# Performance work log

Hardware: AMD Instinct MI355X
Metric: run time of the kernel (lower is better)

The kernel has to match this reference:

```python
import jax, jax.numpy as jnp
import numpy as np

L, D, H, N, R = 4, 256, 512, 16, 8  # layers, d_model, hidden=2*d_model, state_dim, dt_rank
OUT_LEN, IN_DIM = 96, 32
EPS = 1e-5


def _layernorm(v, g, b):
    m = jnp.mean(v, axis=-1, keepdims=True)
    var = jnp.mean((v - m) ** 2, axis=-1, keepdims=True)
    return (v - m) / jnp.sqrt(var + EPS) * g + b


def _pos_encoding(T, d):
    pos = jnp.arange(T, dtype=jnp.float32)[:, None]
    div = jnp.exp(jnp.arange(0, d, 2, dtype=jnp.float32) * (-np.log(10000.0) / d))
    pe = jnp.zeros((T, d), dtype=jnp.float32)
    pe = pe.at[:, 0::2].set(jnp.sin(pos * div))
    pe = pe.at[:, 1::2].set(jnp.cos(pos * div))
    return pe


def setup_inputs() -> dict:
    key = jax.random.key(0)
    ks = jax.random.split(key, 20)
    inp = {
        "x": jax.random.normal(ks[0], (8, 1024, IN_DIM), dtype=jnp.float32),
        "emb_w": jax.random.normal(ks[1], (D, IN_DIM), dtype=jnp.float32) * 0.1,
        "emb_b": jnp.zeros((D,), dtype=jnp.float32),
        "norm_g": jnp.ones((L, D), dtype=jnp.float32),
        "norm_b": jnp.zeros((L, D), dtype=jnp.float32),
        "in_w": jax.random.normal(ks[2], (L, H, D), dtype=jnp.float32) * (1.0 / np.sqrt(D)),
        "conv_w": jax.random.normal(ks[3], (L, H, 1, 3), dtype=jnp.float32) * 0.5,
        "A_p": jax.random.normal(ks[4], (L, H, N), dtype=jnp.float32) * 0.01,
        "D_p": jnp.ones((L, H), dtype=jnp.float32),
        "dt1_w": jax.random.normal(ks[5], (L, R, H), dtype=jnp.float32) * (1.0 / np.sqrt(H)),
        "dt1_b": jnp.zeros((L, R), dtype=jnp.float32),
        "dt2_w": jax.random.normal(ks[6], (L, H, R), dtype=jnp.float32) * (1.0 / np.sqrt(R)),
        "dt2_b": jnp.zeros((L, H), dtype=jnp.float32),
        "out_w": jax.random.normal(ks[7], (L, D, H), dtype=jnp.float32) * (1.0 / np.sqrt(H)),
        "final_g": jnp.ones((D,), dtype=jnp.float32),
        "final_b": jnp.zeros((D,), dtype=jnp.float32),
        "head1_w": jax.random.normal(ks[8], (D, D), dtype=jnp.float32) * (1.0 / np.sqrt(D)),
        "head1_b": jnp.zeros((D,), dtype=jnp.float32),
        "head2_w": jax.random.normal(ks[9], (OUT_LEN, D), dtype=jnp.float32) * (1.0 / np.sqrt(D)),
        "head2_b": jnp.zeros((OUT_LEN,), dtype=jnp.float32),
    }
    return inp


def _mamba_block(h, g, b, in_w, conv_w, A_p, D_p, dt1_w, dt1_b, dt2_w, dt2_b, out_w):
    res = h
    v = _layernorm(h, g, b)            # [B,T,D]
    v = jnp.einsum('btd,hd->bth', v, in_w)  # [B,T,H]
    # depthwise conv1d, kernel 3, padding 1, groups=H
    vc = jnp.transpose(v, (0, 2, 1))   # [B,H,T]
    vc = jax.lax.conv_general_dilated(vc, conv_w, window_strides=(1,),
                                      padding=[(1, 1)], feature_group_count=H,
                                      dimension_numbers=('NCH', 'OIH', 'NCH'))
    v = jnp.transpose(jax.nn.silu(vc), (0, 2, 1))  # [B,T,H]
    dt = jax.nn.relu(jnp.einsum('bth,rh->btr', v, dt1_w) + dt1_b)
    dt = jnp.einsum('btr,hr->bth', dt, dt2_w) + dt2_b
    dt = jax.nn.softplus(dt)           # [B,T,H]
    A = -jnp.exp(A_p)                  # [H,N]
    safe_A = jnp.where(jnp.abs(A) < 1e-5, jnp.ones_like(A), A)

    B_sz = v.shape[0]
    state0 = jnp.zeros((B_sz, H, N), dtype=v.dtype)

    def step(state, inp):
        x_t, dt_t = inp  # [B,H] each
        dA = A * dt_t[..., None]            # [B,H,N]
        discA = jnp.exp(dA)
        discB = (discA - 1.0) / safe_A * dt_t[..., None]
        state = discA * state + discB * x_t[..., None]
        y = jnp.einsum('bhn,hn->bh', state, A_p) + D_p * x_t
        return state, y

    xs = (jnp.transpose(v, (1, 0, 2)), jnp.transpose(dt, (1, 0, 2)))  # [T,B,H]
    _, ys = jax.lax.scan(step, state0, xs)
    y = jnp.transpose(ys, (1, 0, 2))   # [B,T,H]
    return res + jnp.einsum('bth,dh->btd', y, out_w)


def reference(x, emb_w, emb_b, norm_g, norm_b, in_w, conv_w, A_p, D_p,
              dt1_w, dt1_b, dt2_w, dt2_b, out_w, final_g, final_b,
              head1_w, head1_b, head2_w, head2_b):
    h = jnp.einsum('bti,di->btd', x, emb_w) + emb_b  # [B,T,D]
    h = h + _pos_encoding(h.shape[1], D)[None]
    for l in range(L):
        h = _mamba_block(h, norm_g[l], norm_b[l], in_w[l], conv_w[l], A_p[l],
                         D_p[l], dt1_w[l], dt1_b[l], dt2_w[l], dt2_b[l], out_w[l])
    h = _layernorm(h, final_g, final_b)
    h = h[:, -1, :]                    # last token [B,D]
    h = jax.nn.silu(h @ head1_w.T + head1_b)
    return h @ head2_w.T + head2_b     # [B, OUT_LEN]
```

## Files before the change

### kernel.cpp

```cpp
#include <hip/hip_runtime.h>
#include <hip/hip_bf16.h>
#include <math.h>

#define BB 8
#define TT 1024
#define DD 256
#define HH 512
#define NN 16
#define RR 8
#define OUT_LEN 96
#define IN_DIM 32
#define MM (BB*TT)

#define SC 16
#define CC (TT/SC)

typedef unsigned short u16;
typedef unsigned int u32;
typedef __attribute__((ext_vector_type(8))) short short8;
typedef __attribute__((ext_vector_type(8))) unsigned short u16x8;
typedef __attribute__((ext_vector_type(4))) float float4v;

__device__ __forceinline__ u16 f2bf(float f) {
    __hip_bfloat16 h = __float2bfloat16(f);
    return *(u16*)&h;
}
__device__ __forceinline__ float bf2f(u16 u) {
    u32 v = ((u32)u) << 16;
    return *(float*)&v;
}

#define GLD_LDS16(src, dst) __builtin_amdgcn_global_load_lds( \
    (const __attribute__((address_space(1))) void*)(src),     \
    (__attribute__((address_space(3))) void*)(dst), 16, 0, 0)

__global__ __launch_bounds__(256) void embed_ln_cvt_kernel(
    const float* __restrict__ x, const float* __restrict__ emb_w,
    const float* __restrict__ emb_b,
    const float* __restrict__ g, const float* __restrict__ b,
    float* __restrict__ h, u16* __restrict__ lnout,
    const float* __restrict__ w_in, u16* __restrict__ wbf_in,
    const float* __restrict__ w_out, u16* __restrict__ wbf_out, int nw)
{
    int bid = blockIdx.x;
    if (bid >= MM) {
        int i = (bid - MM) * 256 + threadIdx.x;
        if (i < nw) wbf_in[i] = f2bf(w_in[i]);
        else        wbf_out[i - nw] = f2bf(w_out[i - nw]);
        return;
    }

    int bt = bid;
    int d  = threadIdx.x;
    int t  = bt & (TT - 1);

    __shared__ float xs[IN_DIM];
    __shared__ float red[4], red2[4];
    if (threadIdx.x < IN_DIM) xs[threadIdx.x] = x[bt * IN_DIM + threadIdx.x];
    __syncthreads();

    const float* w = emb_w + d * IN_DIM;
    float acc = emb_b[d];
#pragma unroll
    for (int i = 0; i < IN_DIM; i++) acc = fmaf(xs[i], w[i], acc);

    int i2 = d & ~1;
    float div = __expf(-(float)i2 * 0.0359778918f);
    float arg = (float)t * div;
    float pe = (d & 1) ? __cosf(arg) : __sinf(arg);
    float val = acc + pe;
    h[bt * DD + d] = val;

    float s = val;
#pragma unroll
    for (int o = 32; o > 0; o >>= 1) s += __shfl_down(s, o);
    int lane = d & 63, wave = d >> 6;
    if (lane == 0) red[wave] = s;
    __syncthreads();
    float mean = (red[0] + red[1] + red[2] + red[3]) * (1.0f / DD);

    float c = val - mean;
    float s2 = c * c;
#pragma unroll
    for (int o = 32; o > 0; o >>= 1) s2 += __shfl_down(s2, o);
    if (lane == 0) red2[wave] = s2;
    __syncthreads();
    float var = (red2[0] + red2[1] + red2[2] + red2[3]) * (1.0f / DD);

    lnout[bt * DD + d] = f2bf(c * rsqrtf(var + 1e-5f) * g[d] + b[d]);
}

template<int BM, int BN, int OUT_BF16>
__global__ __launch_bounds__(256) void gemm_bf16(
    const u16* __restrict__ A, const u16* __restrict__ B,
    void* __restrict__ Cv, int M, int N, int K, int addC)
{
    constexpr int BK = 64;
    constexpr int MT = BM / 32;
    constexpr int NT = BN / 32;
    static_assert(BN == 64, "B staging assumes BN==64");

    __shared__ __align__(16) u16 Al[2][8][BM][8];
    __shared__ __align__(16) u16 Bl[2][8][BN][8];

    const int tid = threadIdx.x;
    const int bm = blockIdx.y * BM;
    const int bn = blockIdx.x * BN;
    const int wid = tid >> 6, lane = tid & 63;
    const int wm = wid >> 1, wn = wid & 1;
    const int lq = lane >> 4, lm = lane & 15;

    float4v acc[MT][NT];
#pragma unroll
    for (int i = 0; i < MT; i++)
#pragma unroll
        for (int j = 0; j < NT; j++) acc[i][j] = (float4v){0.f, 0.f, 0.f, 0.f};

#pragma unroll
    for (int it = 0; it < (8 * BM) / 256; it++) {
        int c = it * 256 + tid;
        int q = c / BM, row = c % BM;
        GLD_LDS16(A + (size_t)(bm + row) * K + q * 8, &Al[0][q][row][0]);
    }
#pragma unroll
    for (int it = 0; it < (8 * BN) / 256; it++) {
        int c = it * 256 + tid;
        int q = c / BN, row = c % BN;
        GLD_LDS16(B + (size_t)(bn + row) * K + q * 8, &Bl[0][q][row][0]);
    }
    __syncthreads();

    int cur = 0;
    for (int k0 = 0; k0 < K; k0 += BK) {
        if (k0 + BK < K) {
            int nxt = cur ^ 1;
#pragma unroll
            for (int it = 0; it < (8 * BM) / 256; it++) {
                int c = it * 256 + tid;
                int q = c / BM, row = c % BM;
                GLD_LDS16(A + (size_t)(bm + row) * K + k0 + BK + q * 8, &Al[nxt][q][row][0]);
            }
#pragma unroll
            for (int it = 0; it < (8 * BN) / 256; it++) {
                int c = it * 256 + tid;
                int q = c / BN, row = c % BN;
                GLD_LDS16(B + (size_t)(bn + row) * K + k0 + BK + q * 8, &Bl[nxt][q][row][0]);
            }
        }

        short8 af[2][MT], bf[2][NT];
#pragma unroll
        for (int kk = 0; kk < 2; kk++) {
#pragma unroll
            for (int mt = 0; mt < MT; mt++)
                af[kk][mt] = *(const short8*)&Al[cur][kk * 4 + lq][wm * (BM / 2) + mt * 16 + lm][0];
#pragma unroll
            for (int nt = 0; nt < NT; nt++)
                bf[kk][nt] = *(const short8*)&Bl[cur][kk * 4 + lq][wn * (BN / 2) + nt * 16 + lm][0];
        }

#pragma unroll
        for (int kk = 0; kk < 2; kk++)
#pragma unroll
            for (int mt = 0; mt < MT; mt++)
#pragma unroll
                for (int nt = 0; nt < NT; nt++)
                    acc[mt][nt] = __builtin_amdgcn_mfma_f32_16x16x32_bf16(
                        af[kk][mt], bf[kk][nt], acc[mt][nt], 0, 0, 0);
        __syncthreads();
        cur ^= 1;
    }

#pragma unroll
    for (int mt = 0; mt < MT; mt++)
#pragma unroll
        for (int nt = 0; nt < NT; nt++) {
            int row0 = bm + wm * (BM / 2) + mt * 16 + lq * 4;
            int col  = bn + wn * (BN / 2) + nt * 16 + lm;
#pragma unroll
            for (int r = 0; r < 4; r++) {
                float vv = acc[mt][nt][r];
                if (OUT_BF16) {
                    ((u16*)Cv)[(size_t)(row0 + r) * N + col] = f2bf(vv);
                } else {
                    float* cp = (float*)Cv + (size_t)(row0 + r) * N + col;
                    if (addC) vv += *cp;
                    *cp = vv;
                }
            }
        }
}

__global__ __launch_bounds__(256) void gemm2_ln(
    const u16* __restrict__ A, const u16* __restrict__ B,
    float* __restrict__ h,
    const float* __restrict__ g, const float* __restrict__ bb,
    u16* __restrict__ lnout, int doLN)
{
    constexpr int BM = 32;
    __shared__ __align__(16) u16 Al[2][8][BM][8];
    __shared__ __align__(16) u16 Bl[2][8][256][8];
    __shared__ float rs[2][BM], qs[2][BM];

    const int tid = threadIdx.x;
    const int bm = blockIdx.x * BM;
    const int wid = tid >> 6, lane = tid & 63;
    const int wm = wid >> 1, wn = wid & 1;
    const int lq = lane >> 4, lm = lane & 15;

    float4v acc[8];
#pragma unroll
    for (int j = 0; j < 8; j++) acc[j] = (float4v){0.f, 0.f, 0.f, 0.f};

    {
        int q = tid >> 5, row = tid & 31;
        GLD_LDS16(A + (size_t)(bm + row) * 512 + q * 8, &Al[0][q][row][0]);
    }
#pragma unroll
    for (int it = 0; it < 8; it++) {
        int c = it * 256 + tid;
        int q = c >> 8, row = c & 255;
        GLD_LDS16(B + (size_t)row * 512 + q * 8, &Bl[0][q][row][0]);
    }
    __syncthreads();

    int cur = 0;
    for (int k0 = 0; k0 < 512; k0 += 64) {
        if (k0 + 64 < 512) {
            int nxt = cur ^ 1;
            {
                int q = tid >> 5, row = tid & 31;
                GLD_LDS16(A + (size_t)(bm + row) * 512 + k0 + 64 + q * 8, &Al[nxt][q][row][0]);
            }
#pragma unroll
            for (int it = 0; it < 8; it++) {
                int c = it * 256 + tid;
                int q = c >> 8, row = c & 255;
                GLD_LDS16(B + (size_t)row * 512 + k0 + 64 + q * 8, &Bl[nxt][q][row][0]);
            }
        }

        short8 af[2], bf[2][8];
#pragma unroll
        for (int kk = 0; kk < 2; kk++) {
            af[kk] = *(const short8*)&Al[cur][kk * 4 + lq][wm * 16 + lm][0];
#pragma unroll
            for (int nt = 0; nt < 8; nt++)
                bf[kk][nt] = *(const short8*)&Bl[cur][kk * 4 + lq][wn * 128 + nt * 16 + lm][0];
        }
#pragma unroll
        for (int kk = 0; kk < 2; kk++)
#pragma unroll
            for (int nt = 0; nt < 8; nt++)
                acc[nt] = __builtin_amdgcn_mfma_f32_16x16x32_bf16(
                    af[kk], bf[kk][nt], acc[nt], 0, 0, 0);
        __syncthreads();
        cur ^= 1;
    }

    float val[4][8];
    float s1[4] = {0.f, 0.f, 0.f, 0.f}, s2[4] = {0.f, 0.f, 0.f, 0.f};
#pragma unroll
    for (int r = 0; r < 4; r++) {
        int row = bm + wm * 16 + lq * 4 + r;
#pragma unroll
        for (int nt = 0; nt < 8; nt++) {
            int col = wn * 128 + nt * 16 + lm;
            float v = acc[nt][r] + h[(size_t)row * DD + col];
            val[r][nt] = v;
            s1[r] += v;
            s2[r] = fmaf(v, v, s2[r]);
            h[(size_t)row * DD + col] = v;
        }
    }
#pragma unroll
    for (int r = 0; r < 4; r++) {
#pragma unroll
        for (int o = 1; o < 16; o <<= 1) {
            s1[r] += __shfl_xor(s1[r], o);
            s2[r] += __shfl_xor(s2[r], o);
        }
    }
    if (lm == 0) {
#pragma unroll
        for (int r = 0; r < 4; r++) {
            rs[wn][wm * 16 + lq * 4 + r] = s1[r];
            qs[wn][wm * 16 + lq * 4 + r] = s2[r];
        }
    }
    __syncthreads();

    if (doLN) {
#pragma unroll
        for (int r = 0; r < 4; r++) {
            int i = wm * 16 + lq * 4 + r;
            int row = bm + i;
            float mean = (rs[0][i] + rs[1][i]) * (1.0f / DD);
            float var  = (qs[0][i] + qs[1][i]) * (1.0f / DD) - mean * mean;
            float rstd = rsqrtf(var + 1e-5f);
#pragma unroll
            for (int nt = 0; nt < 8; nt++) {
                int col = wn * 128 + nt * 16 + lm;
                lnout[(size_t)row * DD + col] =
                    f2bf((val[r][nt] - mean) * rstd * g[col] + bb[col]);
            }
        }
    }
}

__global__ __launch_bounds__(256) void conv_dt1_kernel(
    const u16* __restrict__ v, const float* __restrict__ cwg,
    const float* __restrict__ w1g, const float* __restrict__ b1g,
    u16* __restrict__ vsb, float* __restrict__ dtr)
{
    __shared__ float w1s[RR * 2 * 256];
    int tid = threadIdx.x;
    {
        int lane = tid & 63, rc = tid >> 6;
#pragma unroll
        for (int i = 0; i < 4; i++) {
            int rci = rc + i * 4;
            int r = rci >> 1, jc = rci & 1;
            float4 wv = *(const float4*)(w1g + r * HH + lane * 8 + jc * 4);
            *(float4*)&w1s[rci * 256 + lane * 4] = wv;
        }
    }
    __syncthreads();

    int wave = tid >> 6, lane = tid & 63;
    int m = blockIdx.x * 4 + wave;
    int t = m & (TT - 1);
    int h0 = lane * 8;

    const u16* vrow = v + (size_t)m * HH + h0;
    u16x8 x0 = *(const u16x8*)vrow;
    u16x8 xm = (t > 0)      ? *(const u16x8*)(vrow - HH) : (u16x8)(0);
    u16x8 xp = (t < TT - 1) ? *(const u16x8*)(vrow + HH) : (u16x8)(0);

    const float* wp = cwg + h0 * 3;
    float a[8];
    u16x8 o;
#pragma unroll
    for (int j = 0; j < 8; j++) {
        float s = wp[j * 3] * bf2f(xm[j]);
        s = fmaf(wp[j * 3 + 1], bf2f(x0[j]), s);
        s = fmaf(wp[j * 3 + 2], bf2f(xp[j]), s);
        s = s / (1.0f + __expf(-s));
        a[j] = s;
        o[j] = f2bf(s);
    }
    *(u16x8*)(vsb + (size_t)m * HH + h0) = o;

    float acc[RR];
#pragma unroll
    for (int r = 0; r < RR; r++) {
        float4 wlo = *(const float4*)&w1s[(r * 2 + 0) * 256 + lane * 4];
        float4 whi = *(const float4*)&w1s[(r * 2 + 1) * 256 + lane * 4];
        float s = a[0] * wlo.x;
        s = fmaf(a[1], wlo.y, s);
        s = fmaf(a[2], wlo.z, s);
        s = fmaf(a[3], wlo.w, s);
        s = fmaf(a[4], whi.x, s);
        s = fmaf(a[5], whi.y, s);
        s = fmaf(a[6], whi.z, s);
        s = fmaf(a[7], whi.w, s);
        acc[r] = s;
    }
#pragma unroll
    for (int r = 0; r < RR; r++) {
#pragma unroll
        for (int o2 = 1; o2 < 64; o2 <<= 1) acc[r] += __shfl_xor(acc[r], o2);
    }
    if (lane == 0) {
#pragma unroll
        for (int r = 0; r < RR; r++) acc[r] = fmaxf(acc[r] + b1g[r], 0.0f);
        *(float4*)(dtr + (size_t)m * RR)     = make_float4(acc[0], acc[1], acc[2], acc[3]);
        *(float4*)(dtr + (size_t)m * RR + 4) = make_float4(acc[4], acc[5], acc[6], acc[7]);
    }
}

__device__ __forceinline__ float softplus_f(float s) {
    return (s > 20.0f) ? s : __logf(1.0f + __expf(s));
}

__global__ __launch_bounds__(256, 4) void scan_pass1(
    const u16* __restrict__ vs, const float* __restrict__ dtr,
    const float* __restrict__ dt2_w, const float* __restrict__ dt2_b,
    const float* __restrict__ A_p,
    u16* __restrict__ Lst, float* __restrict__ sdt)
{
    int h = blockIdx.x * 256 + threadIdx.x;
    int c = blockIdx.y;
    int b = blockIdx.z;

    __shared__ float ds[SC * RR];
    {
        const float* drow = dtr + ((size_t)b * TT + (size_t)c * SC) * RR;
        if (threadIdx.x < SC * RR) ds[threadIdx.x] = drow[threadIdx.x];
    }

    float A2[NN], invA[NN], st[NN];
    const float* ap = A_p + h * NN;
#pragma unroll
    for (int n = 0; n < NN; n++) {
        float a = -__expf(ap[n]);
        A2[n] = a * 1.44269504f;
        invA[n] = 1.0f / a;
        st[n] = 0.0f;
    }
    float w2[RR];
#pragma unroll
    for (int r = 0; r < RR; r++) w2[r] = dt2_w[h * RR + r];
    float b2 = dt2_b[h];

    const u16* vbase = vs + ((size_t)b * TT + (size_t)c * SC) * HH + h;
    float xv = bf2f(vbase[0]);
    __syncthreads();

    float s_dt = 0.0f;
#pragma unroll 2
    for (int t = 0; t < SC; t++) {
        float xn = (t + 1 < SC) ? bf2f(vbase[(size_t)(t + 1) * HH]) : 0.0f;
        float s = b2;
#pragma unroll
        for (int r = 0; r < RR; r++) s = fmaf(ds[t * RR + r], w2[r], s);
        float dt = softplus_f(s);
        s_dt += dt;
        float dtx = dt * xv;
#pragma unroll
        for (int n = 0; n < NN; n++) {
            float e = __builtin_amdgcn_exp2f(A2[n] * dt);
            float u = invA[n] * dtx;
            st[n] = fmaf(e, st[n] + u, -u);
        }
        xv = xn;
    }

    size_t base = (((size_t)c * BB + b) * HH + h) * NN;
    u16x8 lo, hi;
#pragma unroll
    for (int n = 0; n < 8; n++) { lo[n] = f2bf(st[n]); hi[n] = f2bf(st[n + 8]); }
    *(u16x8*)(Lst + base)     = lo;
    *(u16x8*)(Lst + base + 8) = hi;
    sdt[((size_t)c * BB + b) * HH + h] = s_dt;
}

__global__ __launch_bounds__(256) void scan_carry_par(
    const float* __restrict__ A_p, const float* __restrict__ sdt,
    u16* __restrict__ Lst)
{
    int gw   = (blockIdx.x << 2) | (threadIdx.x >> 6);
    int lane = threadIdx.x & 63;
    int b = gw >> 9;
    int h = gw & 511;

    size_t sidx = ((size_t)lane * BB + b) * HH + h;
    float sd = sdt[sidx];
    const float* ap = A_p + h * NN;
    u16x8 Llo = *(const u16x8*)(Lst + sidx * NN);
    u16x8 Lhi = *(const u16x8*)(Lst + sidx * NN + 8);
    u16x8 Elo, Ehi;
#pragma unroll
    for (int n = 0; n < NN; n++) {
        float An = -__expf(ap[n]);
        float p  = __expf(An * sd);
        float lv = bf2f((n < 8) ? Llo[n] : Lhi[n - 8]);
#pragma unroll
        for (int d2 = 1; d2 < 64; d2 <<= 1) {
            float pp = __shfl_up(p, d2);
            float pl = __shfl_up(lv, d2);
            if (lane >= d2) { lv = fmaf(pl, p, lv); p = pp * p; }
        }
        float E = __shfl_up(lv, 1);
        if (lane == 0) E = 0.0f;
        if (n < 8) Elo[n] = f2bf(E); else Ehi[n - 8] = f2bf(E);
    }
    *(u16x8*)(Lst + sidx * NN)     = Elo;
    *(u16x8*)(Lst + sidx * NN + 8) = Ehi;
}

__global__ __launch_bounds__(256, 4) void scan_pass2(
    const u16* __restrict__ vs,
    const float* __restrict__ dtr,
    const float* __restrict__ dt2_w,
    const float* __restrict__ dt2_b,
    const float* __restrict__ A_p, const float* __restrict__ D_p,
    const u16* __restrict__ carry,
    u16* __restrict__ y)
{
    int h = blockIdx.x * 256 + threadIdx.x;
    int c = blockIdx.y;
    int b = blockIdx.z;

    __shared__ float ds[SC * RR];
    {
        const float* drow = dtr + ((size_t)b * TT + (size_t)c * SC) * RR;
        if (threadIdx.x < SC * RR) ds[threadIdx.x] = drow[threadIdx.x];
    }

    float A2[NN], invA[NN], Ap[NN], st[NN];
    const float* app = A_p + h * NN;
    size_t cbase = (((size_t)c * BB + b) * HH + h) * NN;
    {
        u16x8 lo = *(const u16x8*)(carry + cbase);
        u16x8 hi = *(const u16x8*)(carry + cbase + 8);
#pragma unroll
        for (int n = 0; n < 8; n++) { st[n] = bf2f(lo[n]); st[n + 8] = bf2f(hi[n]); }
    }
#pragma unroll
    for (int n = 0; n < NN; n++) {
        float apv = app[n];
        Ap[n] = apv;
        float a = -__expf(apv);
        A2[n] = a * 1.44269504f;
        invA[n] = 1.0f / a;
    }
    float w2[RR];
#pragma unroll
    for (int r = 0; r < RR; r++) w2[r] = dt2_w[h * RR + r];
    float b2 = dt2_b[h];
    float Dp = D_p[h];

    const u16* vbase = vs + ((size_t)b * TT + (size_t)c * SC) * HH + h;
    u16*       ybase = y  + ((size_t)b * TT + (size_t)c * SC) * HH + h;
    float xv = bf2f(vbase[0]);
    __syncthreads();

#pragma unroll 2
    for (int t = 0; t < SC; t++) {
        float xn = (t + 1 < SC) ? bf2f(vbase[(size_t)(t + 1) * HH]) : 0.0f;
        float s = b2;
#pragma unroll
        for (int r = 0; r < RR; r++) s = fmaf(ds[t * RR + r], w2[r], s);
        float dt = softplus_f(s);
        float dtx = dt * xv;
        float acc = Dp * xv;
#pragma unroll
        for (int n = 0; n < NN; n++) {
            float e = __builtin_amdgcn_exp2f(A2[n] * dt);
            float u = invA[n] * dtx;
            st[n] = fmaf(e, st[n] + u, -u);
            acc = fmaf(st[n], Ap[n], acc);
        }
        ybase[(size_t)t * HH] = f2bf(acc);
        xv = xn;
    }
}

__global__ __launch_bounds__(256) void head_kernel(
    const float* __restrict__ h,
    const float* __restrict__ fg, const float* __restrict__ fb,
    const float* __restrict__ w1, const float* __restrict__ b1,
    const float* __restrict__ w2, const float* __restrict__ b2,
    float* __restrict__ out)
{
    int b = blockIdx.x;
    int d = threadIdx.x;
    __shared__ float hn[DD], s1[DD];
    __shared__ float red[4];

    float v = h[((size_t)b * TT + (TT - 1)) * DD + d];

    float s = v;
#pragma unroll
    for (int o = 32; o > 0; o >>= 1) s += __shfl_down(s, o);
    int lane = d & 63, wave = d >> 6;
    if (lane == 0) red[wave] = s;
    __syncthreads();
    float mean = (red[0] + red[1] + red[2] + red[3]) * (1.0f / DD);
    __syncthreads();

    float c = v - mean;
    float s2 = c * c;
#pragma unroll
    for (int o = 32; o > 0; o >>= 1) s2 += __shfl_down(s2, o);
    if (lane == 0) red[wave] = s2;
    __syncthreads();
    float var = (red[0] + red[1] + red[2] + red[3]) * (1.0f / DD);

    hn[d] = c * rsqrtf(var + 1e-5f) * fg[d] + fb[d];
    __syncthreads();

    float a1 = b1[d];
    const float* w1r = w1 + d * DD;
#pragma unroll 8
    for (int k = 0; k < DD; k++) a1 = fmaf(hn[k], w1r[k], a1);
    s1[d] = a1 / (1.0f + __expf(-a1));
    __syncthreads();

    if (d < OUT_LEN) {
        float a2 = b2[d];
        const float* w2r = w2 + d * DD;
#pragma unroll 8
        for (int k = 0; k < DD; k++) a2 = fmaf(s1[k], w2r[k], a2);
        out[b * OUT_LEN + d] = a2;
    }
}

extern "C" void kernel_launch(void* const* d_in, const int* in_sizes, int n_in,
                              void* d_out, int out_size, void* d_ws, size_t ws_size,
                              hipStream_t stream)
{
    (void)in_sizes; (void)n_in; (void)out_size; (void)ws_size;

    const float* x       = (const float*)d_in[0];
    const float* emb_w   = (const float*)d_in[1];
    const float* emb_b   = (const float*)d_in[2];
    const float* norm_g  = (const float*)d_in[3];
    const float* norm_b  = (const float*)d_in[4];
    const float* in_w    = (const float*)d_in[5];
    const float* conv_w  = (const float*)d_in[6];
    const float* A_p     = (const float*)d_in[7];
    const float* D_p     = (const float*)d_in[8];
    const float* dt1_w   = (const float*)d_in[9];
    const float* dt1_b   = (const float*)d_in[10];
    const float* dt2_w   = (const float*)d_in[11];
    const float* dt2_b   = (const float*)d_in[12];
    const float* out_w   = (const float*)d_in[13];
    const float* final_g = (const float*)d_in[14];
    const float* final_b = (const float*)d_in[15];
    const float* head1_w = (const float*)d_in[16];
    const float* head1_b = (const float*)d_in[17];
    const float* head2_w = (const float*)d_in[18];
    const float* head2_b = (const float*)d_in[19];
    float* outp = (float*)d_out;

    char* ws = (char*)d_ws;
    float* h     = (float*)ws;                ws += (size_t)MM * DD * 4;
    u16*   vbf   = (u16*)ws;                  ws += (size_t)MM * HH * 2;
    u16*   vsb   = (u16*)ws;                  ws += (size_t)MM * HH * 2;
    u16*   ybf   = (u16*)ws;                  ws += (size_t)MM * HH * 2;
    u16*   lnbuf = (u16*)ws;                  ws += (size_t)MM * DD * 2;
    float* dtr   = (float*)ws;                ws += (size_t)MM * RR * 4;
    u16*   Lst   = (u16*)ws;                  ws += (size_t)CC * BB * HH * NN * 2;
    float* sdt   = (float*)ws;                ws += (size_t)CC * BB * HH * 4;
    u16*   wbf_in  = (u16*)ws;                ws += (size_t)4 * HH * DD * 2;
    u16*   wbf_out = (u16*)ws;                ws += (size_t)4 * DD * HH * 2;

    const int NW = 4 * HH * DD;
    embed_ln_cvt_kernel<<<MM + (2 * NW) / 256, 256, 0, stream>>>(
        x, emb_w, emb_b, norm_g, norm_b, h, lnbuf,
        in_w, wbf_in, out_w, wbf_out, NW);

    for (int l = 0; l < 4; l++) {
        gemm_bf16<128, 64, 1><<<dim3(HH / 64, MM / 128), 256, 0, stream>>>(
            lnbuf, wbf_in + (size_t)l * HH * DD, vbf, MM, HH, DD, 0);
        conv_dt1_kernel<<<MM / 4, 256, 0, stream>>>(
            vbf, conv_w + (size_t)l * HH * 3,
            dt1_w + (size_t)l * RR * HH, dt1_b + l * RR, vsb, dtr);

        scan_pass1<<<dim3(HH / 256, CC, BB), 256, 0, stream>>>(
            vsb, dtr, dt2_w + (size_t)l * HH * RR, dt2_b + l * HH,
            A_p + (size_t)l * HH * NN, Lst, sdt);
        scan_carry_par<<<(BB * HH) / 4, 256, 0, stream>>>(
            A_p + (size_t)l * HH * NN, sdt, Lst);
        scan_pass2<<<dim3(HH / 256, CC, BB), 256, 0, stream>>>(
            vsb, dtr, dt2_w + (size_t)l * HH * RR, dt2_b + l * HH,
            A_p + (size_t)l * HH * NN, D_p + l * HH, Lst, ybf);

        const float* g_next = (l < 3) ? (norm_g + (l + 1) * DD) : final_g;
        const float* b_next = (l < 3) ? (norm_b + (l + 1) * DD) : final_b;
        gemm2_ln<<<MM / 32, 256, 0, stream>>>(
            ybf, wbf_out + (size_t)l * DD * HH, h, g_next, b_next,
            lnbuf, (l < 3) ? 1 : 0);
    }

    head_kernel<<<BB, 256, 0, stream>>>(h, final_g, final_b,
                                        head1_w, head1_b, head2_w, head2_b, outp);
}
```

Baseline: 498.8 us.

## Fuse conv/dt1 into scan pass1 and use vmcnt-based waits in GEMMs

Merges the depthwise conv + SiLU + dt1 projection kernel into the first chunked-scan pass. Each 512-thread block now computes one chunk's conv outputs and stages them in LDS, so the scan reads its inputs from LDS instead of global memory, and one launch is removed per layer. Separately, both GEMM kernels replace __syncthreads with explicit s_waitcnt vmcnt(N) plus s_barrier, so the next tile's loads can stay in flight while the current tile is consumed. The hardcoded vmcnt counts tie the GEMM code to specific tile shapes. The fused kernel also runs only 64x8 blocks of 512 threads, which lowers parallelism for the conv part.

New measurement: 485.7 us. 2.6% less time.

```diff
diff --git a/kernel.cpp b/kernel.cpp
--- a/kernel.cpp
+++ b/kernel.cpp
@@ -34,6 +34,11 @@
     (const __attribute__((address_space(1))) void*)(src),     \
     (__attribute__((address_space(3))) void*)(dst), 16, 0, 0)
 
+#define SBAR()   asm volatile("s_barrier" ::: "memory")
+#define VMCNT0() asm volatile("s_waitcnt vmcnt(0)" ::: "memory")
+#define VMCNT6() asm volatile("s_waitcnt vmcnt(6)" ::: "memory")
+#define VMCNT9() asm volatile("s_waitcnt vmcnt(9)" ::: "memory")
+
 __global__ __launch_bounds__(256) void embed_ln_cvt_kernel(
     const float* __restrict__ x, const float* __restrict__ emb_w,
     const float* __restrict__ emb_b,
@@ -98,7 +103,7 @@
     constexpr int BK = 64;
     constexpr int MT = BM / 32;
     constexpr int NT = BN / 32;
-    static_assert(BN == 64, "B staging assumes BN==64");
+    static_assert(BM == 128 && BN == 64, "vmcnt count assumes 6 loads/thread");
 
     __shared__ __align__(16) u16 Al[2][8][BM][8];
     __shared__ __align__(16) u16 Bl[2][8][BN][8];
@@ -128,25 +133,30 @@
         int q = c / BN, row = c % BN;
         GLD_LDS16(B + (size_t)(bn + row) * K + q * 8, &Bl[0][q][row][0]);
     }
-    __syncthreads();
-
+
+    const int nt = K / BK;
     int cur = 0;
-    for (int k0 = 0; k0 < K; k0 += BK) {
-        if (k0 + BK < K) {
+    for (int i = 0; i < nt; i++) {
+        if (i + 1 < nt) {
             int nxt = cur ^ 1;
+            int k1 = (i + 1) * BK;
 #pragma unroll
             for (int it = 0; it < (8 * BM) / 256; it++) {
                 int c = it * 256 + tid;
                 int q = c / BM, row = c % BM;
-                GLD_LDS16(A + (size_t)(bm + row) * K + k0 + BK + q * 8, &Al[nxt][q][row][0]);
+                GLD_LDS16(A + (size_t)(bm + row) * K + k1 + q * 8, &Al[nxt][q][row][0]);
             }
 #pragma unroll
             for (int it = 0; it < (8 * BN) / 256; it++) {
                 int c = it * 256 + tid;
                 int q = c / BN, row = c % BN;
-                GLD_LDS16(B + (size_t)(bn + row) * K + k0 + BK + q * 8, &Bl[nxt][q][row][0]);
+                GLD_LDS16(B + (size_t)(bn + row) * K + k1 + q * 8, &Bl[nxt][q][row][0]);
             }
-        }
+            VMCNT6();
+        } else {
+            VMCNT0();
+        }
+        SBAR();
 
         short8 af[2][MT], bf[2][NT];
 #pragma unroll
@@ -155,8 +165,8 @@
             for (int mt = 0; mt < MT; mt++)
                 af[kk][mt] = *(const short8*)&Al[cur][kk * 4 + lq][wm * (BM / 2) + mt * 16 + lm][0];
 #pragma unroll
-            for (int nt = 0; nt < NT; nt++)
-                bf[kk][nt] = *(const short8*)&Bl[cur][kk * 4 + lq][wn * (BN / 2) + nt * 16 + lm][0];
+            for (int nt2 = 0; nt2 < NT; nt2++)
+                bf[kk][nt2] = *(const short8*)&Bl[cur][kk * 4 + lq][wn * (BN / 2) + nt2 * 16 + lm][0];
         }
 
 #pragma unroll
@@ -164,22 +174,22 @@
 #pragma unroll
             for (int mt = 0; mt < MT; mt++)
 #pragma unroll
-                for (int nt = 0; nt < NT; nt++)
-                    acc[mt][nt] = __builtin_amdgcn_mfma_f32_16x16x32_bf16(
-                        af[kk][mt], bf[kk][nt], acc[mt][nt], 0, 0, 0);
-        __syncthreads();
+                for (int nt2 = 0; nt2 < NT; nt2++)
+                    acc[mt][nt2] = __builtin_amdgcn_mfma_f32_16x16x32_bf16(
+                        af[kk][mt], bf[kk][nt2], acc[mt][nt2], 0, 0, 0);
+        SBAR();
         cur ^= 1;
     }
 
 #pragma unroll
     for (int mt = 0; mt < MT; mt++)
 #pragma unroll
-        for (int nt = 0; nt < NT; nt++) {
+        for (int nt2 = 0; nt2 < NT; nt2++) {
             int row0 = bm + wm * (BM / 2) + mt * 16 + lq * 4;
-            int col  = bn + wn * (BN / 2) + nt * 16 + lm;
+            int col  = bn + wn * (BN / 2) + nt2 * 16 + lm;
 #pragma unroll
             for (int r = 0; r < 4; r++) {
-                float vv = acc[mt][nt][r];
+                float vv = acc[mt][nt2][r];
                 if (OUT_BF16) {
                     ((u16*)Cv)[(size_t)(row0 + r) * N + col] = f2bf(vv);
                 } else {
@@ -222,23 +232,27 @@
         int q = c >> 8, row = c & 255;
         GLD_LDS16(B + (size_t)row * 512 + q * 8, &Bl[0][q][row][0]);
     }
-    __syncthreads();
 
     int cur = 0;
-    for (int k0 = 0; k0 < 512; k0 += 64) {
-        if (k0 + 64 < 512) {
+    for (int i = 0; i < 8; i++) {
+        if (i + 1 < 8) {
             int nxt = cur ^ 1;
+            int k1 = (i + 1) * 64;
             {
                 int q = tid >> 5, row = tid & 31;
-                GLD_LDS16(A + (size_t)(bm + row) * 512 + k0 + 64 + q * 8, &Al[nxt][q][row][0]);
+                GLD_LDS16(A + (size_t)(bm + row) * 512 + k1 + q * 8, &Al[nxt][q][row][0]);
             }
 #pragma unroll
             for (int it = 0; it < 8; it++) {
                 int c = it * 256 + tid;
                 int q = c >> 8, row = c & 255;
-                GLD_LDS16(B + (size_t)row * 512 + k0 + 64 + q * 8, &Bl[nxt][q][row][0]);
+                GLD_LDS16(B + (size_t)row * 512 + k1 + q * 8, &Bl[nxt][q][row][0]);
             }
-        }
+            VMCNT9();
+        } else {
+            VMCNT0();
+        }
+        SBAR();
 
         short8 af[2], bf[2][8];
 #pragma unroll
@@ -254,7 +268,7 @@
             for (int nt = 0; nt < 8; nt++)
                 acc[nt] = __builtin_amdgcn_mfma_f32_16x16x32_bf16(
                     af[kk], bf[kk][nt], acc[nt], 0, 0, 0);
-        __syncthreads();
+        SBAR();
         cur ^= 1;
     }
 
@@ -308,104 +322,102 @@
     }
 }
 
-__global__ __launch_bounds__(256) void conv_dt1_kernel(
-    const u16* __restrict__ v, const float* __restrict__ cwg,
-    const float* __restrict__ w1g, const float* __restrict__ b1g,
-    u16* __restrict__ vsb, float* __restrict__ dtr)
-{
-    __shared__ float w1s[RR * 2 * 256];
-    int tid = threadIdx.x;
-    {
-        int lane = tid & 63, rc = tid >> 6;
-#pragma unroll
-        for (int i = 0; i < 4; i++) {
-            int rci = rc + i * 4;
-            int r = rci >> 1, jc = rci & 1;
-            float4 wv = *(const float4*)(w1g + r * HH + lane * 8 + jc * 4);
-            *(float4*)&w1s[rci * 256 + lane * 4] = wv;
-        }
-    }
-    __syncthreads();
-
-    int wave = tid >> 6, lane = tid & 63;
-    int m = blockIdx.x * 4 + wave;
-    int t = m & (TT - 1);
-    int h0 = lane * 8;
-
-    const u16* vrow = v + (size_t)m * HH + h0;
-    u16x8 x0 = *(const u16x8*)vrow;
-    u16x8 xm = (t > 0)      ? *(const u16x8*)(vrow - HH) : (u16x8)(0);
-    u16x8 xp = (t < TT - 1) ? *(const u16x8*)(vrow + HH) : (u16x8)(0);
-
-    const float* wp = cwg + h0 * 3;
-    float a[8];
-    u16x8 o;
-#pragma unroll
-    for (int j = 0; j < 8; j++) {
-        float s = wp[j * 3] * bf2f(xm[j]);
-        s = fmaf(wp[j * 3 + 1], bf2f(x0[j]), s);
-        s = fmaf(wp[j * 3 + 2], bf2f(xp[j]), s);
-        s = s / (1.0f + __expf(-s));
-        a[j] = s;
-        o[j] = f2bf(s);
-    }
-    *(u16x8*)(vsb + (size_t)m * HH + h0) = o;
-
-    float acc[RR];
-#pragma unroll
-    for (int r = 0; r < RR; r++) {
-        float4 wlo = *(const float4*)&w1s[(r * 2 + 0) * 256 + lane * 4];
-        float4 whi = *(const float4*)&w1s[(r * 2 + 1) * 256 + lane * 4];
-        float s = a[0] * wlo.x;
-        s = fmaf(a[1], wlo.y, s);
-        s = fmaf(a[2], wlo.z, s);
-        s = fmaf(a[3], wlo.w, s);
-        s = fmaf(a[4], whi.x, s);
-        s = fmaf(a[5], whi.y, s);
-        s = fmaf(a[6], whi.z, s);
-        s = fmaf(a[7], whi.w, s);
-        acc[r] = s;
-    }
-#pragma unroll
-    for (int r = 0; r < RR; r++) {
-#pragma unroll
-        for (int o2 = 1; o2 < 64; o2 <<= 1) acc[r] += __shfl_xor(acc[r], o2);
-    }
-    if (lane == 0) {
-#pragma unroll
-        for (int r = 0; r < RR; r++) acc[r] = fmaxf(acc[r] + b1g[r], 0.0f);
-        *(float4*)(dtr + (size_t)m * RR)     = make_float4(acc[0], acc[1], acc[2], acc[3]);
-        *(float4*)(dtr + (size_t)m * RR + 4) = make_float4(acc[4], acc[5], acc[6], acc[7]);
-    }
-}
-
 __device__ __forceinline__ float softplus_f(float s) {
     return (s > 20.0f) ? s : __logf(1.0f + __expf(s));
 }
 
-__global__ __launch_bounds__(256, 4) void scan_pass1(
-    const u16* __restrict__ vs, const float* __restrict__ dtr,
+__global__ __launch_bounds__(512, 4) void conv_scan1(
+    const u16* __restrict__ vbf, const float* __restrict__ cwg,
+    const float* __restrict__ w1g, const float* __restrict__ b1g,
     const float* __restrict__ dt2_w, const float* __restrict__ dt2_b,
     const float* __restrict__ A_p,
+    u16* __restrict__ vsb, float* __restrict__ dtr,
     u16* __restrict__ Lst, float* __restrict__ sdt)
 {
-    int h = blockIdx.x * 256 + threadIdx.x;
-    int c = blockIdx.y;
-    int b = blockIdx.z;
-
+    const int c = blockIdx.x;
+    const int b = blockIdx.y;
+    const int tid = threadIdx.x;
+    const int wave = tid >> 6, lane = tid & 63;
+    const int h0 = lane * 8;
+
+    __shared__ float w1s[RR * 2 * 256];
+    __shared__ u16   a_lds[SC][HH];
     __shared__ float ds[SC * RR];
-    {
-        const float* drow = dtr + ((size_t)b * TT + (size_t)c * SC) * RR;
-        if (threadIdx.x < SC * RR) ds[threadIdx.x] = drow[threadIdx.x];
-    }
-
+
+#pragma unroll
+    for (int i = 0; i < 2; i++) {
+        int rci = wave + i * 8;
+        int r = rci >> 1, jc = rci & 1;
+        float4 wv = *(const float4*)(w1g + r * HH + lane * 8 + jc * 4);
+        *(float4*)&w1s[rci * 256 + lane * 4] = wv;
+    }
+    __syncthreads();
+
+    const float* wp = cwg + h0 * 3;
+#pragma unroll
+    for (int i = 0; i < 2; i++) {
+        int tr = wave + i * 8;
+        int t  = c * SC + tr;
+        size_t m = (size_t)b * TT + t;
+
+        const u16* vrow = vbf + m * HH + h0;
+        u16x8 x0 = *(const u16x8*)vrow;
+        u16x8 xm = (t > 0)      ? *(const u16x8*)(vrow - HH) : (u16x8)(0);
+        u16x8 xp = (t < TT - 1) ? *(const u16x8*)(vrow + HH) : (u16x8)(0);
+
+        float a[8];
+        u16x8 o;
+#pragma unroll
+        for (int j = 0; j < 8; j++) {
+            float s = wp[j * 3] * bf2f(xm[j]);
+            s = fmaf(wp[j * 3 + 1], bf2f(x0[j]), s);
+            s = fmaf(wp[j * 3 + 2], bf2f(xp[j]), s);
+            s = s / (1.0f + __expf(-s));
+            a[j] = s;
+            o[j] = f2bf(s);
+        }
+        *(u16x8*)(vsb + m * HH + h0) = o;
+        *(u16x8*)&a_lds[tr][h0]      = o;
+
+        float acc[RR];
+#pragma unroll
+        for (int r = 0; r < RR; r++) {
+            float4 wlo = *(const float4*)&w1s[(r * 2 + 0) * 256 + lane * 4];
+            float4 whi = *(const float4*)&w1s[(r * 2 + 1) * 256 + lane * 4];
+            float s = a[0] * wlo.x;
+            s = fmaf(a[1], wlo.y, s);
+            s = fmaf(a[2], wlo.z, s);
+            s = fmaf(a[3], wlo.w, s);
+            s = fmaf(a[4], whi.x, s);
+            s = fmaf(a[5], whi.y, s);
+            s = fmaf(a[6], whi.z, s);
+            s = fmaf(a[7], whi.w, s);
+            acc[r] = s;
+        }
+#pragma unroll
+        for (int r = 0; r < RR; r++) {
+#pragma unroll
+            for (int o2 = 1; o2 < 64; o2 <<= 1) acc[r] += __shfl_xor(acc[r], o2);
+        }
+        if (lane == 0) {
+#pragma unroll
+            for (int r = 0; r < RR; r++) acc[r] = fmaxf(acc[r] + b1g[r], 0.0f);
+            *(float4*)(dtr + m * RR)     = make_float4(acc[0], acc[1], acc[2], acc[3]);
+            *(float4*)(dtr + m * RR + 4) = make_float4(acc[4], acc[5], acc[6], acc[7]);
+#pragma unroll
+            for (int r = 0; r < RR; r++) ds[tr * RR + r] = acc[r];
+        }
+    }
+    __syncthreads();
+
+    const int h = tid;
     float A2[NN], invA[NN], st[NN];
     const float* ap = A_p + h * NN;
 #pragma unroll
     for (int n = 0; n < NN; n++) {
-        float a = -__expf(ap[n]);
-        A2[n] = a * 1.44269504f;
-        invA[n] = 1.0f / a;
+        float av = -__expf(ap[n]);
+        A2[n] = av * 1.44269504f;
+        invA[n] = 1.0f / av;
         st[n] = 0.0f;
     }
     float w2[RR];
@@ -413,14 +425,11 @@
     for (int r = 0; r < RR; r++) w2[r] = dt2_w[h * RR + r];
     float b2 = dt2_b[h];
 
-    const u16* vbase = vs + ((size_t)b * TT + (size_t)c * SC) * HH + h;
-    float xv = bf2f(vbase[0]);
-    __syncthreads();
-
+    float xv = bf2f(a_lds[0][h]);
     float s_dt = 0.0f;
 #pragma unroll 2
     for (int t = 0; t < SC; t++) {
-        float xn = (t + 1 < SC) ? bf2f(vbase[(size_t)(t + 1) * HH]) : 0.0f;
+        float xn = (t + 1 < SC) ? bf2f(a_lds[t + 1][h]) : 0.0f;
         float s = b2;
 #pragma unroll
         for (int r = 0; r < RR; r++) s = fmaf(ds[t * RR + r], w2[r], s);
@@ -645,15 +654,17 @@
     for (int l = 0; l < 4; l++) {
         gemm_bf16<128, 64, 1><<<dim3(HH / 64, MM / 128), 256, 0, stream>>>(
             lnbuf, wbf_in + (size_t)l * HH * DD, vbf, MM, HH, DD, 0);
-        conv_dt1_kernel<<<MM / 4, 256, 0, stream>>>(
+
+        conv_scan1<<<dim3(CC, BB), 512, 0, stream>>>(
             vbf, conv_w + (size_t)l * HH * 3,
-            dt1_w + (size_t)l * RR * HH, dt1_b + l * RR, vsb, dtr);
-
-        scan_pass1<<<dim3(HH / 256, CC, BB), 256, 0, stream>>>(
-            vsb, dtr, dt2_w + (size_t)l * HH * RR, dt2_b + l * HH,
-            A_p + (size_t)l * HH * NN, Lst, sdt);
+            dt1_w + (size_t)l * RR * HH, dt1_b + l * RR,
+            dt2_w + (size_t)l * HH * RR, dt2_b + l * HH,
+            A_p + (size_t)l * HH * NN,
+            vsb, dtr, Lst, sdt);
+
         scan_carry_par<<<(BB * HH) / 4, 256, 0, stream>>>(
             A_p + (size_t)l * HH * NN, sdt, Lst);
+
         scan_pass2<<<dim3(HH / 256, CC, BB), 256, 0, stream>>>(
             vsb, dtr, dt2_w + (size_t)l * HH * RR, dt2_b + l * HH,
             A_p + (size_t)l * HH * NN, D_p + l * HH, Lst, ybf);
```
